# Optimization experiments

Hardware: AMD Instinct MI355X
Metric: run time of the kernel (lower is better)

## Reference

```python
import jax, jax.numpy as jnp
import numpy as np

N = 100_000   # nodes
E = 1_600_000 # edges (avg degree 16)
F_IN, H1, H2, H3, C = 32, 32, 32, 16, 8


def _gcn_conv(h, W, b, src, dst, norm):
    # h: [N, Fin] -> project then normalized sparse aggregate (PyG GCNConv)
    h = h @ W                                   # [N, Fout]
    msg = h[src] * norm[:, None]                # gather + scale, [E', Fout]
    agg = jax.ops.segment_sum(msg, dst, num_segments=N)
    return agg + b


def setup_inputs() -> dict:
    key = jax.random.key(0)
    ks = jax.random.split(key, 8)
    x = jax.random.normal(ks[0], (N, F_IN), dtype=jnp.float32)
    edge_index = jax.random.randint(ks[1], (2, E), 0, N, dtype=jnp.int64)
    def w(k, fi, fo):
        return jax.random.normal(k, (fi, fo), dtype=jnp.float32) / np.float32(np.sqrt(fi))
    return {
        "x": x,
        "edge_index": edge_index,
        "W1": w(ks[2], F_IN, H1), "b1": jnp.zeros((H1,), jnp.float32),
        "W2": w(ks[3], H1, H2),   "b2": jnp.zeros((H2,), jnp.float32),
        "W3": w(ks[4], H2, H3),   "b3": jnp.zeros((H3,), jnp.float32),
        "Wc": w(ks[5], H3, C),    "bc": jnp.zeros((C,), jnp.float32),
    }


def reference(x, edge_index, W1, b1, W2, b2, W3, b3, Wc, bc):
    src, dst = edge_index[0], edge_index[1]
    loops = jnp.arange(N, dtype=src.dtype)
    src_f = jnp.concatenate([src, loops])       # add self-loops
    dst_f = jnp.concatenate([dst, loops])
    # symmetric normalization D^-1/2 (A+I) D^-1/2 (deg over targets, incl. self-loop)
    deg = jax.ops.segment_sum(jnp.ones_like(dst_f, dtype=x.dtype), dst_f, num_segments=N)
    dinv = jax.lax.rsqrt(deg)                   # deg >= 1 due to self-loops
    norm = dinv[src_f] * dinv[dst_f]            # [E+N]

    h = jnp.tanh(_gcn_conv(x, W1, b1, src_f, dst_f, norm))
    h = jnp.tanh(_gcn_conv(h, W2, b2, src_f, dst_f, norm))
    h = jnp.tanh(_gcn_conv(h, W3, b3, src_f, dst_f, norm))
    out = h @ Wc + bc
    return (out, h)
```

## Files before the change

kernel.cpp:

```cpp
#include <hip/hip_runtime.h>

static constexpr int NN = 100000;
static constexpr int NE = 1600000;

static constexpr int BSH   = 9;
static constexpr int NDB   = 1 << BSH;
static constexpr int NBUCK = (NN + NDB - 1) / NDB;
static constexpr int BCAP  = 9216;
static constexpr int BSTRIDE = BCAP + NDB * 15;
static constexpr int TILE  = 4096;
static constexpr int BIN_T = 256;
static constexpr int EPT   = TILE / BIN_T;

static_assert(NBUCK <= 256, "bucket count must fit one block");
static_assert(NN % 32 == 0, "node-group kernels assume divisibility");


__global__ void k_init_cur(int* __restrict__ gcur) {
    const int t = threadIdx.x;
    if (t < NBUCK) gcur[t] = t * BCAP;
}

__global__ __launch_bounds__(BIN_T) void k_bin(const int* __restrict__ src,
                                               const int* __restrict__ dst,
                                               int* __restrict__ gcur,
                                               unsigned* __restrict__ bkt) {
    __shared__ int hist[NBUCK];
    __shared__ int cur[NBUCK];
    const int t = threadIdx.x;
    const int e0 = blockIdx.x * TILE;
    const int n = (NE - e0 < TILE) ? (NE - e0) : TILE;
    for (int i = t; i < NBUCK; i += BIN_T) hist[i] = 0;
    __syncthreads();
    unsigned rec[EPT];
    int bb[EPT];
#pragma unroll
    for (int j = 0; j < EPT; ++j) {
        const int i = t + j * BIN_T;
        bb[j] = -1;
        if (i < n) {
            const int s = src[e0 + i];
            const int d = dst[e0 + i];
            bb[j] = d >> BSH;
            rec[j] = ((unsigned)s << BSH) | (unsigned)(d & (NDB - 1));
            atomicAdd(&hist[bb[j]], 1);
        }
    }
    __syncthreads();
    for (int i = t; i < NBUCK; i += BIN_T) {
        const int c = hist[i];
        cur[i] = (c > 0) ? atomicAdd(&gcur[i], c) : 0;
    }
    __syncthreads();
#pragma unroll
    for (int j = 0; j < EPT; ++j) {
        if (bb[j] >= 0) {
            const int pos = atomicAdd(&cur[bb[j]], 1);
            bkt[pos] = rec[j];
        }
    }
}

__global__ __launch_bounds__(256) void k_build(const unsigned* __restrict__ bkt,
                                               const int* __restrict__ gcur,
                                               int* __restrict__ csr,
                                               int* __restrict__ npad,
                                               int* __restrict__ offs,
                                               float* __restrict__ dinv) {
    __shared__ unsigned buf[BCAP];
    __shared__ int hist[NDB];
    __shared__ int sc[NDB];
    __shared__ int cur[NDB];
    const int b = blockIdx.x;
    const int t = threadIdx.x;
    const int n0 = b << BSH;
    const int nn = (NN - n0 < NDB) ? (NN - n0) : NDB;
    const int base = b * BSTRIDE;
    int cnt = gcur[b] - b * BCAP;
    if (cnt > BCAP) cnt = BCAP;
    for (int i = t; i < NDB; i += 256) hist[i] = 0;
    __syncthreads();
    for (int i = t; i < cnt; i += 256) {
        const unsigned r = bkt[(size_t)b * BCAP + i];
        buf[i] = r;
        atomicAdd(&hist[r & (NDB - 1)], 1);
    }
    __syncthreads();
    sc[t] = (hist[t] + 15) & ~15;
    sc[t + 256] = (hist[t + 256] + 15) & ~15;
    __syncthreads();
    for (int off = 1; off < NDB; off <<= 1) {
        const int a0 = (t >= off) ? sc[t - off] : 0;
        const int a1 = (t + 256 >= off) ? sc[t + 256 - off] : 0;
        __syncthreads();
        sc[t] += a0;
        sc[t + 256] += a1;
        __syncthreads();
    }
    for (int i = t; i < NDB; i += 256) {
        const int h = hist[i];
        const int lp = (h + 15) & ~15;
        const int e = sc[i] - lp;
        cur[i] = e;
        if (i < nn) {
            const int node = n0 + i;
            npad[node] = lp;
            offs[node] = base + e;
            dinv[node] = rsqrtf((float)h + 1.0f);
            for (int j = h; j < lp; ++j) csr[base + e + j] = NN;
        }
    }
    __syncthreads();
    for (int i = t; i < cnt; i += 256) {
        const unsigned r = buf[i];
        const int pos = atomicAdd(&cur[r & (NDB - 1)], 1);
        csr[base + pos] = (int)(r >> BSH);
    }
}


template <int FIN, int FOUT>
__global__ __launch_bounds__(256) void k_proj(const float* __restrict__ in,
                                              const float* __restrict__ W,
                                              const float* __restrict__ dinv,
                                              float* __restrict__ p) {
    constexpr int NPB = 256 / FOUT;
    __shared__ float Ws[FIN * FOUT];
    __shared__ float rows[NPB][FIN];
    const int tid = threadIdx.x;
    if (blockIdx.x == 0 && tid < FOUT) p[(size_t)NN * FOUT + tid] = 0.f;
    for (int i = tid; i < FIN * FOUT; i += 256) Ws[i] = W[i];
    const int nl = tid / FOUT;
    const int f = tid % FOUT;
    const int node = blockIdx.x * NPB + nl;
    if (node < NN) {
        for (int k = f; k < FIN; k += FOUT) rows[nl][k] = in[(size_t)node * FIN + k];
    }
    __syncthreads();
    if (node >= NN) return;
    float acc = 0.f;
#pragma unroll
    for (int k = 0; k < FIN; ++k) acc += rows[nl][k] * Ws[k * FOUT + f];
    p[(size_t)node * FOUT + f] = acc * dinv[node];
}

template <int FOUT>
__global__ __launch_bounds__(256) void k_agg_proj(const float2* __restrict__ p2,
                                                  const int* __restrict__ offs,
                                                  const int* __restrict__ npad,
                                                  const float* __restrict__ dinv,
                                                  const int* __restrict__ csr,
                                                  const float2* __restrict__ bias2,
                                                  const float* __restrict__ W,
                                                  float* __restrict__ pout) {
    constexpr int LPN = 16;
    constexpr int NPB = 256 / LPN;
    constexpr int OPL = FOUT / LPN;
    __shared__ float Ws[32 * FOUT];
    __shared__ float hs[NPB][33];
    const int tid = threadIdx.x;
    if (blockIdx.x == 0 && tid < FOUT) pout[(size_t)NN * FOUT + tid] = 0.f;
    for (int i = tid; i < 32 * FOUT; i += 256) Ws[i] = W[i];
    const int nl = tid / LPN;
    const int f2 = tid % LPN;
    const int node = blockIdx.x * NPB + nl;
    const int start = offs[node];
    const int L = npad[node];
    const float2 self = p2[(size_t)node * LPN + f2];
    float ax = self.x, ay = self.y;
    for (int kk = 0; kk < L; kk += 16) {
        const int* cp = csr + start + kk;
        int s[16];
#pragma unroll
        for (int j = 0; j < 16; ++j) s[j] = cp[j];
        float2 v[16];
#pragma unroll
        for (int j = 0; j < 16; ++j) v[j] = p2[(size_t)s[j] * LPN + f2];
        float sx0 = 0.f, sy0 = 0.f, sx1 = 0.f, sy1 = 0.f;
#pragma unroll
        for (int j = 0; j < 8; ++j) {
            sx0 += v[j].x; sy0 += v[j].y;
            sx1 += v[j + 8].x; sy1 += v[j + 8].y;
        }
        ax += sx0 + sx1;
        ay += sy0 + sy1;
    }
    const float di = dinv[node];
    const float2 bb = bias2[f2];
    const float hx = tanhf(di * ax + bb.x);
    const float hy = tanhf(di * ay + bb.y);
    hs[nl][2 * f2] = hx;
    hs[nl][2 * f2 + 1] = hy;
    __syncthreads();
    float acc[OPL];
#pragma unroll
    for (int o = 0; o < OPL; ++o) acc[o] = 0.f;
#pragma unroll
    for (int k = 0; k < 32; ++k) {
        const float hv = hs[nl][k];
#pragma unroll
        for (int o = 0; o < OPL; ++o) acc[o] += hv * Ws[k * FOUT + f2 * OPL + o];
    }
    if (OPL == 2) {
        float2 r;
        r.x = acc[0] * di;
        r.y = acc[OPL - 1] * di;
        reinterpret_cast<float2*>(pout)[(size_t)node * (FOUT / 2) + f2] = r;
    } else {
        pout[(size_t)node * FOUT + f2] = acc[0] * di;
    }
}

__global__ __launch_bounds__(256) void k_agg_cls(const float2* __restrict__ p2,
                                                 const int* __restrict__ offs,
                                                 const int* __restrict__ npad,
                                                 const float* __restrict__ dinv,
                                                 const int* __restrict__ csr,
                                                 const float2* __restrict__ bias2,
                                                 const float* __restrict__ Wc,
                                                 const float* __restrict__ bc,
                                                 float2* __restrict__ h2out,
                                                 float* __restrict__ out) {
    constexpr int LPN = 8;
    constexpr int NPB = 256 / LPN;
    __shared__ float WcS[16 * 8];
    __shared__ float bcS[8];
    __shared__ float hs[NPB][17];
    const int tid = threadIdx.x;
    if (tid < 128) WcS[tid] = Wc[tid];
    if (tid < 8) bcS[tid] = bc[tid];
    const int nl = tid / LPN;
    const int f2 = tid % LPN;
    const int node = blockIdx.x * NPB + nl;
    const int start = offs[node];
    const int L = npad[node];
    const float2 self = p2[(size_t)node * LPN + f2];
    float ax = self.x, ay = self.y;
    for (int kk = 0; kk < L; kk += 16) {
        const int* cp = csr + start + kk;
        int s[16];
#pragma unroll
        for (int j = 0; j < 16; ++j) s[j] = cp[j];
        float2 v[16];
#pragma unroll
        for (int j = 0; j < 16; ++j) v[j] = p2[(size_t)s[j] * LPN + f2];
        float sx0 = 0.f, sy0 = 0.f, sx1 = 0.f, sy1 = 0.f;
#pragma unroll
        for (int j = 0; j < 8; ++j) {
            sx0 += v[j].x; sy0 += v[j].y;
            sx1 += v[j + 8].x; sy1 += v[j + 8].y;
        }
        ax += sx0 + sx1;
        ay += sy0 + sy1;
    }
    const float di = dinv[node];
    const float2 bb = bias2[f2];
    const float hx = tanhf(di * ax + bb.x);
    const float hy = tanhf(di * ay + bb.y);
    h2out[(size_t)node * LPN + f2] = make_float2(hx, hy);
    hs[nl][2 * f2] = hx;
    hs[nl][2 * f2 + 1] = hy;
    __syncthreads();
    float acc = bcS[f2];
#pragma unroll
    for (int k = 0; k < 16; ++k) acc += hs[nl][k] * WcS[k * 8 + f2];
    out[(size_t)node * 8 + f2] = acc;
}


extern "C" void kernel_launch(void* const* d_in, const int* in_sizes, int n_in,
                              void* d_out, int out_size, void* d_ws, size_t ws_size,
                              hipStream_t stream) {
    const float* x  = (const float*)d_in[0];
    const int*   ei = (const int*)d_in[1];
    const float* W1 = (const float*)d_in[2];
    const float* b1 = (const float*)d_in[3];
    const float* W2 = (const float*)d_in[4];
    const float* b2 = (const float*)d_in[5];
    const float* W3 = (const float*)d_in[6];
    const float* b3 = (const float*)d_in[7];
    const float* Wc = (const float*)d_in[8];
    const float* bc = (const float*)d_in[9];

    const int* src = ei;
    const int* dst = ei + NE;

    int*   gcur = (int*)d_ws;
    int*   npad = gcur + 256;
    int*   offs = npad + NN;
    float* dinv = (float*)(offs + NN);
    int*   csr  = (int*)(dinv + NN);
    float* B0   = (float*)(csr + (size_t)NBUCK * BSTRIDE);
    float* B1   = B0 + (size_t)(NN + 1) * 32;
    unsigned* bkt = (unsigned*)B0;

    float* out = (float*)d_out;
    float* h3  = out + (size_t)NN * 8;

    const int T = 256;

    k_init_cur<<<1, T, 0, stream>>>(gcur);
    k_bin<<<(NE + TILE - 1) / TILE, BIN_T, 0, stream>>>(src, dst, gcur, bkt);
    k_build<<<NBUCK, T, 0, stream>>>(bkt, gcur, csr, npad, offs, dinv);

    k_proj<32, 32><<<NN / 8, T, 0, stream>>>(x, W1, dinv, B0);

    k_agg_proj<32><<<NN / 16, T, 0, stream>>>((const float2*)B0, offs, npad, dinv, csr,
                                              (const float2*)b1, W2, B1);

    k_agg_proj<16><<<NN / 16, T, 0, stream>>>((const float2*)B1, offs, npad, dinv, csr,
                                              (const float2*)b2, W3, B0);

    k_agg_cls<<<NN / 32, T, 0, stream>>>((const float2*)B0, offs, npad, dinv, csr,
                                         (const float2*)b3, Wc, bc,
                                         (float2*)h3, out);
}
```

Before: 164.2 us.

## Fuse binning with layer-1 projection, split CSR build per half-bucket, widen gathers to float4

The edge binning kernel and the first dense projection now run as one launch, with extra blocks doing x@W1. The dinv scaling of that projection moves into the CSR build, which is split into two blocks per bucket so each handles 256 nodes. The cursor init kernel is replaced by a memset. The aggregation kernels now gather float4 per lane instead of float2, using fewer lanes per node and more nodes per block. This removes two launches and raises parallelism in the build, at the cost of each build block scanning the whole bucket twice and an extra read-modify-write pass over B0.

Result: faster. 151.7 us (-7.6%).

```diff
diff --git a/kernel.cpp b/kernel.cpp
--- a/kernel.cpp
+++ b/kernel.cpp
@@ -7,57 +7,71 @@
 static constexpr int NDB   = 1 << BSH;
 static constexpr int NBUCK = (NN + NDB - 1) / NDB;
 static constexpr int BCAP  = 9216;
-static constexpr int BSTRIDE = BCAP + NDB * 15;
+static constexpr int HSTRIDE = 8704;
+static constexpr int BSTRIDE = 2 * HSTRIDE;
 static constexpr int TILE  = 4096;
-static constexpr int BIN_T = 256;
-static constexpr int EPT   = TILE / BIN_T;
+static constexpr int NBIN  = (NE + TILE - 1) / TILE;
+static constexpr int EPT   = TILE / 256;
 
 static_assert(NBUCK <= 256, "bucket count must fit one block");
-static_assert(NN % 32 == 0, "node-group kernels assume divisibility");
-
-
-__global__ void k_init_cur(int* __restrict__ gcur) {
+
+__global__ __launch_bounds__(256) void k_bin_proj(const int* __restrict__ src,
+                                                  const int* __restrict__ dst,
+                                                  int* __restrict__ gcur,
+                                                  unsigned* __restrict__ bkt,
+                                                  const float* __restrict__ x,
+                                                  const float* __restrict__ W1,
+                                                  float* __restrict__ p) {
     const int t = threadIdx.x;
-    if (t < NBUCK) gcur[t] = t * BCAP;
-}
-
-__global__ __launch_bounds__(BIN_T) void k_bin(const int* __restrict__ src,
-                                               const int* __restrict__ dst,
-                                               int* __restrict__ gcur,
-                                               unsigned* __restrict__ bkt) {
-    __shared__ int hist[NBUCK];
-    __shared__ int cur[NBUCK];
-    const int t = threadIdx.x;
-    const int e0 = blockIdx.x * TILE;
-    const int n = (NE - e0 < TILE) ? (NE - e0) : TILE;
-    for (int i = t; i < NBUCK; i += BIN_T) hist[i] = 0;
-    __syncthreads();
-    unsigned rec[EPT];
-    int bb[EPT];
-#pragma unroll
-    for (int j = 0; j < EPT; ++j) {
-        const int i = t + j * BIN_T;
-        bb[j] = -1;
-        if (i < n) {
-            const int s = src[e0 + i];
-            const int d = dst[e0 + i];
-            bb[j] = d >> BSH;
-            rec[j] = ((unsigned)s << BSH) | (unsigned)(d & (NDB - 1));
-            atomicAdd(&hist[bb[j]], 1);
-        }
-    }
-    __syncthreads();
-    for (int i = t; i < NBUCK; i += BIN_T) {
-        const int c = hist[i];
-        cur[i] = (c > 0) ? atomicAdd(&gcur[i], c) : 0;
-    }
-    __syncthreads();
-#pragma unroll
-    for (int j = 0; j < EPT; ++j) {
-        if (bb[j] >= 0) {
-            const int pos = atomicAdd(&cur[bb[j]], 1);
-            bkt[pos] = rec[j];
-        }
+    if (blockIdx.x < NBIN) {
+        __shared__ int hist[NBUCK];
+        __shared__ int cur[NBUCK];
+        const int e0 = blockIdx.x * TILE;
+        const int n = (NE - e0 < TILE) ? (NE - e0) : TILE;
+        for (int i = t; i < NBUCK; i += 256) hist[i] = 0;
+        __syncthreads();
+        unsigned rec[EPT];
+        int bb[EPT];
+#pragma unroll
+        for (int j = 0; j < EPT; ++j) {
+            const int i = t + j * 256;
+            bb[j] = -1;
+            if (i < n) {
+                const int s = src[e0 + i];
+                const int d = dst[e0 + i];
+                bb[j] = d >> BSH;
+                rec[j] = ((unsigned)s << BSH) | (unsigned)(d & (NDB - 1));
+                atomicAdd(&hist[bb[j]], 1);
+            }
+        }
+        __syncthreads();
+        for (int i = t; i < NBUCK; i += 256) {
+            const int c = hist[i];
+            cur[i] = (c > 0) ? (i * BCAP + atomicAdd(&gcur[i], c)) : 0;
+        }
+        __syncthreads();
+#pragma unroll
+        for (int j = 0; j < EPT; ++j) {
+            if (bb[j] >= 0) {
+                const int pos = atomicAdd(&cur[bb[j]], 1);
+                bkt[pos] = rec[j];
+            }
+        }
+    } else {
+        __shared__ float Ws[1024];
+        __shared__ float rows[8][33];
+        const int pb = blockIdx.x - NBIN;
+        if (pb == 0 && t < 32) p[(size_t)NN * 32 + t] = 0.f;
+        for (int i = t; i < 1024; i += 256) Ws[i] = W1[i];
+        const int nl = t >> 5;
+        const int f = t & 31;
+        const int node = pb * 8 + nl;
+        rows[nl][f] = x[(size_t)node * 32 + f];
+        __syncthreads();
+        float acc = 0.f;
+#pragma unroll
+        for (int k = 0; k < 32; ++k) acc += rows[nl][k] * Ws[k * 32 + f];
+        p[(size_t)node * 32 + f] = acc;
     }
 }
 
@@ -66,131 +80,115 @@
                                                int* __restrict__ csr,
                                                int* __restrict__ npad,
                                                int* __restrict__ offs,
-                                               float* __restrict__ dinv) {
-    __shared__ unsigned buf[BCAP];
-    __shared__ int hist[NDB];
-    __shared__ int sc[NDB];
-    __shared__ int cur[NDB];
-    const int b = blockIdx.x;
+                                               float* __restrict__ dinv,
+                                               float* __restrict__ B0) {
+    __shared__ int hist[256];
+    __shared__ int sc[256];
+    __shared__ int cur[256];
+    const int bb = blockIdx.x;
+    const int b = bb >> 1;
+    const unsigned half = bb & 1;
+    const int h0 = (b << BSH) + (int)half * 256;
+    const int nh = (NN - h0 < 256) ? (NN - h0) : 256;
     const int t = threadIdx.x;
-    const int n0 = b << BSH;
-    const int nn = (NN - n0 < NDB) ? (NN - n0) : NDB;
-    const int base = b * BSTRIDE;
-    int cnt = gcur[b] - b * BCAP;
+    int cnt = gcur[b];
     if (cnt > BCAP) cnt = BCAP;
-    for (int i = t; i < NDB; i += 256) hist[i] = 0;
-    __syncthreads();
-    for (int i = t; i < cnt; i += 256) {
-        const unsigned r = bkt[(size_t)b * BCAP + i];
-        buf[i] = r;
-        atomicAdd(&hist[r & (NDB - 1)], 1);
-    }
-    __syncthreads();
-    sc[t] = (hist[t] + 15) & ~15;
-    sc[t + 256] = (hist[t + 256] + 15) & ~15;
-    __syncthreads();
-    for (int off = 1; off < NDB; off <<= 1) {
-        const int a0 = (t >= off) ? sc[t - off] : 0;
-        const int a1 = (t + 256 >= off) ? sc[t + 256 - off] : 0;
-        __syncthreads();
-        sc[t] += a0;
-        sc[t + 256] += a1;
-        __syncthreads();
-    }
-    for (int i = t; i < NDB; i += 256) {
-        const int h = hist[i];
-        const int lp = (h + 15) & ~15;
-        const int e = sc[i] - lp;
-        cur[i] = e;
-        if (i < nn) {
-            const int node = n0 + i;
-            npad[node] = lp;
-            offs[node] = base + e;
-            dinv[node] = rsqrtf((float)h + 1.0f);
-            for (int j = h; j < lp; ++j) csr[base + e + j] = NN;
-        }
-    }
-    __syncthreads();
-    for (int i = t; i < cnt; i += 256) {
-        const unsigned r = buf[i];
-        const int pos = atomicAdd(&cur[r & (NDB - 1)], 1);
-        csr[base + pos] = (int)(r >> BSH);
-    }
-}
-
-
-template <int FIN, int FOUT>
-__global__ __launch_bounds__(256) void k_proj(const float* __restrict__ in,
-                                              const float* __restrict__ W,
-                                              const float* __restrict__ dinv,
-                                              float* __restrict__ p) {
-    constexpr int NPB = 256 / FOUT;
-    __shared__ float Ws[FIN * FOUT];
-    __shared__ float rows[NPB][FIN];
-    const int tid = threadIdx.x;
-    if (blockIdx.x == 0 && tid < FOUT) p[(size_t)NN * FOUT + tid] = 0.f;
-    for (int i = tid; i < FIN * FOUT; i += 256) Ws[i] = W[i];
-    const int nl = tid / FOUT;
-    const int f = tid % FOUT;
-    const int node = blockIdx.x * NPB + nl;
-    if (node < NN) {
-        for (int k = f; k < FIN; k += FOUT) rows[nl][k] = in[(size_t)node * FIN + k];
-    }
-    __syncthreads();
-    if (node >= NN) return;
-    float acc = 0.f;
-#pragma unroll
-    for (int k = 0; k < FIN; ++k) acc += rows[nl][k] * Ws[k * FOUT + f];
-    p[(size_t)node * FOUT + f] = acc * dinv[node];
+    hist[t] = 0;
+    __syncthreads();
+    const unsigned* bp = bkt + (size_t)b * BCAP;
+    if (nh > 0) {
+        for (int i = t; i < cnt; i += 256) {
+            const unsigned r = bp[i];
+            if (((r >> 8) & 1u) == half) atomicAdd(&hist[r & 255], 1);
+        }
+    }
+    __syncthreads();
+    const int h = hist[t];
+    const int lp = (h + 15) & ~15;
+    sc[t] = lp;
+    __syncthreads();
+    for (int off = 1; off < 256; off <<= 1) {
+        const int a = (t >= off) ? sc[t - off] : 0;
+        __syncthreads();
+        sc[t] += a;
+        __syncthreads();
+    }
+    const int rbase = b * BSTRIDE + (int)half * HSTRIDE;
+    const int e = rbase + (sc[t] - lp);
+    cur[t] = e;
+    if (t < nh) {
+        const int node = h0 + t;
+        npad[node] = lp;
+        offs[node] = e;
+        dinv[node] = rsqrtf((float)h + 1.0f);
+        for (int j = h; j < lp; ++j) csr[e + j] = NN;
+    }
+    __syncthreads();
+    if (nh > 0) {
+        for (int i = t; i < cnt; i += 256) {
+            const unsigned r = bp[i];
+            if (((r >> 8) & 1u) == half) {
+                const int pos = atomicAdd(&cur[r & 255], 1);
+                csr[pos] = (int)(r >> BSH);
+            }
+        }
+        float4* B04 = (float4*)B0;
+        for (int i = t; i < nh * 8; i += 256) {
+            const int node = h0 + (i >> 3);
+            const float di = dinv[node];
+            float4 v = B04[(size_t)node * 8 + (i & 7)];
+            v.x *= di; v.y *= di; v.z *= di; v.w *= di;
+            B04[(size_t)node * 8 + (i & 7)] = v;
+        }
+    }
 }
 
 template <int FOUT>
-__global__ __launch_bounds__(256) void k_agg_proj(const float2* __restrict__ p2,
+__global__ __launch_bounds__(256) void k_agg_proj(const float4* __restrict__ p4,
                                                   const int* __restrict__ offs,
                                                   const int* __restrict__ npad,
                                                   const float* __restrict__ dinv,
                                                   const int* __restrict__ csr,
-                                                  const float2* __restrict__ bias2,
+                                                  const float4* __restrict__ bias4,
                                                   const float* __restrict__ W,
                                                   float* __restrict__ pout) {
-    constexpr int LPN = 16;
-    constexpr int NPB = 256 / LPN;
-    constexpr int OPL = FOUT / LPN;
+    constexpr int NPB = 32;
+    constexpr int OPL = FOUT / 8;
     __shared__ float Ws[32 * FOUT];
     __shared__ float hs[NPB][33];
     const int tid = threadIdx.x;
     if (blockIdx.x == 0 && tid < FOUT) pout[(size_t)NN * FOUT + tid] = 0.f;
     for (int i = tid; i < 32 * FOUT; i += 256) Ws[i] = W[i];
-    const int nl = tid / LPN;
-    const int f2 = tid % LPN;
+    const int nl = tid >> 3;
+    const int f4 = tid & 7;
     const int node = blockIdx.x * NPB + nl;
     const int start = offs[node];
     const int L = npad[node];
-    const float2 self = p2[(size_t)node * LPN + f2];
-    float ax = self.x, ay = self.y;
+    const float4 self = p4[(size_t)node * 8 + f4];
+    float ax = self.x, ay = self.y, az = self.z, aw = self.w;
     for (int kk = 0; kk < L; kk += 16) {
         const int* cp = csr + start + kk;
         int s[16];
 #pragma unroll
         for (int j = 0; j < 16; ++j) s[j] = cp[j];
-        float2 v[16];
-#pragma unroll
-        for (int j = 0; j < 16; ++j) v[j] = p2[(size_t)s[j] * LPN + f2];
-        float sx0 = 0.f, sy0 = 0.f, sx1 = 0.f, sy1 = 0.f;
+        float4 v[16];
+#pragma unroll
+        for (int j = 0; j < 16; ++j) v[j] = p4[(size_t)s[j] * 8 + f4];
+        float sx0 = 0.f, sy0 = 0.f, sz0 = 0.f, sw0 = 0.f;
+        float sx1 = 0.f, sy1 = 0.f, sz1 = 0.f, sw1 = 0.f;
 #pragma unroll
         for (int j = 0; j < 8; ++j) {
-            sx0 += v[j].x; sy0 += v[j].y;
-            sx1 += v[j + 8].x; sy1 += v[j + 8].y;
-        }
-        ax += sx0 + sx1;
-        ay += sy0 + sy1;
+            sx0 += v[j].x; sy0 += v[j].y; sz0 += v[j].z; sw0 += v[j].w;
+            sx1 += v[j + 8].x; sy1 += v[j + 8].y; sz1 += v[j + 8].z; sw1 += v[j + 8].w;
+        }
+        ax += sx0 + sx1; ay += sy0 + sy1; az += sz0 + sz1; aw += sw0 + sw1;
     }
     const float di = dinv[node];
-    const float2 bb = bias2[f2];
-    const float hx = tanhf(di * ax + bb.x);
-    const float hy = tanhf(di * ay + bb.y);
-    hs[nl][2 * f2] = hx;
-    hs[nl][2 * f2 + 1] = hy;
+    const float4 bb = bias4[f4];
+    hs[nl][4 * f4 + 0] = tanhf(di * ax + bb.x);
+    hs[nl][4 * f4 + 1] = tanhf(di * ay + bb.y);
+    hs[nl][4 * f4 + 2] = tanhf(di * az + bb.z);
+    hs[nl][4 * f4 + 3] = tanhf(di * aw + bb.w);
     __syncthreads();
     float acc[OPL];
 #pragma unroll
@@ -199,72 +197,82 @@
     for (int k = 0; k < 32; ++k) {
         const float hv = hs[nl][k];
 #pragma unroll
-        for (int o = 0; o < OPL; ++o) acc[o] += hv * Ws[k * FOUT + f2 * OPL + o];
-    }
-    if (OPL == 2) {
+        for (int o = 0; o < OPL; ++o) acc[o] += hv * Ws[k * FOUT + f4 * OPL + o];
+    }
+    if (OPL == 4) {
+        float4 r;
+        r.x = acc[0] * di; r.y = acc[1] * di; r.z = acc[2] * di; r.w = acc[OPL - 1] * di;
+        reinterpret_cast<float4*>(pout)[(size_t)node * 8 + f4] = r;
+    } else {
         float2 r;
-        r.x = acc[0] * di;
-        r.y = acc[OPL - 1] * di;
-        reinterpret_cast<float2*>(pout)[(size_t)node * (FOUT / 2) + f2] = r;
-    } else {
-        pout[(size_t)node * FOUT + f2] = acc[0] * di;
-    }
-}
-
-__global__ __launch_bounds__(256) void k_agg_cls(const float2* __restrict__ p2,
+        r.x = acc[0] * di; r.y = acc[OPL - 1] * di;
+        reinterpret_cast<float2*>(pout)[(size_t)node * 8 + f4] = r;
+    }
+}
+
+__global__ __launch_bounds__(256) void k_agg_cls(const float4* __restrict__ p4,
                                                  const int* __restrict__ offs,
                                                  const int* __restrict__ npad,
                                                  const float* __restrict__ dinv,
                                                  const int* __restrict__ csr,
-                                                 const float2* __restrict__ bias2,
+                                                 const float4* __restrict__ bias4,
                                                  const float* __restrict__ Wc,
                                                  const float* __restrict__ bc,
-                                                 float2* __restrict__ h2out,
+                                                 float4* __restrict__ h4out,
                                                  float* __restrict__ out) {
-    constexpr int LPN = 8;
-    constexpr int NPB = 256 / LPN;
+    constexpr int NPB = 64;
     __shared__ float WcS[16 * 8];
     __shared__ float bcS[8];
     __shared__ float hs[NPB][17];
     const int tid = threadIdx.x;
     if (tid < 128) WcS[tid] = Wc[tid];
     if (tid < 8) bcS[tid] = bc[tid];
-    const int nl = tid / LPN;
-    const int f2 = tid % LPN;
-    const int node = blockIdx.x * NPB + nl;
+    const int nl = tid >> 2;
+    const int f4 = tid & 3;
+    int node = blockIdx.x * NPB + nl;
+    if (node >= NN) node = NN - 1;
     const int start = offs[node];
     const int L = npad[node];
-    const float2 self = p2[(size_t)node * LPN + f2];
-    float ax = self.x, ay = self.y;
+    const float4 self = p4[(size_t)node * 4 + f4];
+    float ax = self.x, ay = self.y, az = self.z, aw = self.w;
     for (int kk = 0; kk < L; kk += 16) {
         const int* cp = csr + start + kk;
         int s[16];
 #pragma unroll
         for (int j = 0; j < 16; ++j) s[j] = cp[j];
-        float2 v[16];
-#pragma unroll
-        for (int j = 0; j < 16; ++j) v[j] = p2[(size_t)s[j] * LPN + f2];
-        float sx0 = 0.f, sy0 = 0.f, sx1 = 0.f, sy1 = 0.f;
+        float4 v[16];
+#pragma unroll
+        for (int j = 0; j < 16; ++j) v[j] = p4[(size_t)s[j] * 4 + f4];
+        float sx0 = 0.f, sy0 = 0.f, sz0 = 0.f, sw0 = 0.f;
+        float sx1 = 0.f, sy1 = 0.f, sz1 = 0.f, sw1 = 0.f;
 #pragma unroll
         for (int j = 0; j < 8; ++j) {
-            sx0 += v[j].x; sy0 += v[j].y;
-            sx1 += v[j + 8].x; sy1 += v[j + 8].y;
-        }
-        ax += sx0 + sx1;
-        ay += sy0 + sy1;
+            sx0 += v[j].x; sy0 += v[j].y; sz0 += v[j].z; sw0 += v[j].w;
+            sx1 += v[j + 8].x; sy1 += v[j + 8].y; sz1 += v[j + 8].z; sw1 += v[j + 8].w;
+        }
+        ax += sx0 + sx1; ay += sy0 + sy1; az += sz0 + sz1; aw += sw0 + sw1;
     }
     const float di = dinv[node];
-    const float2 bb = bias2[f2];
-    const float hx = tanhf(di * ax + bb.x);
-    const float hy = tanhf(di * ay + bb.y);
-    h2out[(size_t)node * LPN + f2] = make_float2(hx, hy);
-    hs[nl][2 * f2] = hx;
-    hs[nl][2 * f2 + 1] = hy;
-    __syncthreads();
-    float acc = bcS[f2];
-#pragma unroll
-    for (int k = 0; k < 16; ++k) acc += hs[nl][k] * WcS[k * 8 + f2];
-    out[(size_t)node * 8 + f2] = acc;
+    const float4 bb = bias4[f4];
+    float4 h;
+    h.x = tanhf(di * ax + bb.x);
+    h.y = tanhf(di * ay + bb.y);
+    h.z = tanhf(di * az + bb.z);
+    h.w = tanhf(di * aw + bb.w);
+    h4out[(size_t)node * 4 + f4] = h;
+    hs[nl][4 * f4 + 0] = h.x;
+    hs[nl][4 * f4 + 1] = h.y;
+    hs[nl][4 * f4 + 2] = h.z;
+    hs[nl][4 * f4 + 3] = h.w;
+    __syncthreads();
+    float a0 = bcS[2 * f4], a1 = bcS[2 * f4 + 1];
+#pragma unroll
+    for (int k = 0; k < 16; ++k) {
+        const float hv = hs[nl][k];
+        a0 += hv * WcS[k * 8 + 2 * f4];
+        a1 += hv * WcS[k * 8 + 2 * f4 + 1];
+    }
+    reinterpret_cast<float2*>(out)[(size_t)node * 4 + f4] = make_float2(a0, a1);
 }
 
 
@@ -292,26 +300,26 @@
     int*   csr  = (int*)(dinv + NN);
     float* B0   = (float*)(csr + (size_t)NBUCK * BSTRIDE);
     float* B1   = B0 + (size_t)(NN + 1) * 32;
-    unsigned* bkt = (unsigned*)B0;
+    unsigned* bkt = (unsigned*)B1;
 
     float* out = (float*)d_out;
     float* h3  = out + (size_t)NN * 8;
 
     const int T = 256;
 
-    k_init_cur<<<1, T, 0, stream>>>(gcur);
-    k_bin<<<(NE + TILE - 1) / TILE, BIN_T, 0, stream>>>(src, dst, gcur, bkt);
-    k_build<<<NBUCK, T, 0, stream>>>(bkt, gcur, csr, npad, offs, dinv);
-
-    k_proj<32, 32><<<NN / 8, T, 0, stream>>>(x, W1, dinv, B0);
-
-    k_agg_proj<32><<<NN / 16, T, 0, stream>>>((const float2*)B0, offs, npad, dinv, csr,
-                                              (const float2*)b1, W2, B1);
-
-    k_agg_proj<16><<<NN / 16, T, 0, stream>>>((const float2*)B1, offs, npad, dinv, csr,
-                                              (const float2*)b2, W3, B0);
-
-    k_agg_cls<<<NN / 32, T, 0, stream>>>((const float2*)B0, offs, npad, dinv, csr,
-                                         (const float2*)b3, Wc, bc,
-                                         (float2*)h3, out);
-}
+    hipMemsetAsync(gcur, 0, NBUCK * sizeof(int), stream);
+
+    k_bin_proj<<<NBIN + NN / 8, T, 0, stream>>>(src, dst, gcur, bkt, x, W1, B0);
+
+    k_build<<<2 * NBUCK, T, 0, stream>>>(bkt, gcur, csr, npad, offs, dinv, B0);
+
+    k_agg_proj<32><<<NN / 32, T, 0, stream>>>((const float4*)B0, offs, npad, dinv, csr,
+                                              (const float4*)b1, W2, B1);
+
+    k_agg_proj<16><<<NN / 32, T, 0, stream>>>((const float4*)B1, offs, npad, dinv, csr,
+                                              (const float4*)b2, W3, B0);
+
+    k_agg_cls<<<(NN + 63) / 64, T, 0, stream>>>((const float4*)B0, offs, npad, dinv, csr,
+                                                (const float4*)b3, Wc, bc,
+                                                (float4*)h3, out);
+}
```
